# Performance work log

Hardware: AMD Instinct MI355X
Metric: run time of the kernel (lower is better)

The kernel has to match this reference:

```python
import jax, jax.numpy as jnp
import numpy as np

K = 1024
D = 256
BETA = 0.25


def setup_inputs() -> dict:
    key = jax.random.key(0)
    k1, k2 = jax.random.split(key)
    latents = jax.random.normal(k1, (32, D, 32, 32), dtype=jnp.float32)
    # nn.Embedding init: uniform(-1/K, 1/K)
    embedding = jax.random.uniform(k2, (K, D), dtype=jnp.float32,
                                   minval=-1.0 / K, maxval=1.0 / K)
    return {"latents": latents, "embedding": embedding}


def reference(latents, embedding):
    # latents: [B, D, H, W] -> [B, H, W, D]
    x = jnp.transpose(latents, (0, 2, 3, 1))
    input_shape = x.shape
    flat = x.reshape(-1, D)  # [N, D]

    # squared-L2 distances to codebook: [N, K]
    distances = (jnp.sum(flat ** 2, axis=1, keepdims=True)
                 + jnp.sum(embedding ** 2, axis=1)
                 - 2.0 * flat @ embedding.T)
    encoding_indices = jnp.argmin(distances, axis=1)  # [N]

    # one-hot encodings (returned output); quantize via direct gather
    encodings = jax.nn.one_hot(encoding_indices, K, dtype=latents.dtype)  # [N, K]
    quantized = embedding[encoding_indices].reshape(input_shape)  # [B, H, W, D]

    e_latent_loss = jnp.mean((jax.lax.stop_gradient(quantized) - x) ** 2)
    q_latent_loss = jnp.mean((quantized - jax.lax.stop_gradient(x)) ** 2)
    loss = q_latent_loss + BETA * e_latent_loss

    # straight-through estimator
    quantized_st = x + jax.lax.stop_gradient(quantized - x)

    avg_probs = jnp.mean(encodings, axis=0)  # [K]
    perplexity = jnp.exp(-jnp.sum(avg_probs * jnp.log(avg_probs + 1e-10)))

    return (loss,
            jnp.transpose(quantized_st, (0, 3, 1, 2)),  # [B, D, H, W]
            perplexity,
            encodings)
```

## Files before the change

kernel.cpp:

```cpp
#include <hip/hip_runtime.h>
#include <stdint.h>
#include <math.h>

typedef float  f32x4 __attribute__((ext_vector_type(4)));
typedef float  f32x2 __attribute__((ext_vector_type(2)));
typedef short  s16x8 __attribute__((ext_vector_type(8)));
typedef short  s16x4 __attribute__((ext_vector_type(4)));

#define KC   1024
#define DD   256
#define NR   32768

#define WS_HIST   0
#define WS_ACC    4096
#define WS_E2     8192
#define WS_IDX    12288
#define WS_PANEL  143360
#define WS_PART   671744

#define ENC_OFF   8388610ULL

#define A_OFF   0
#define B_OFF   32768
#define E2_OFF  49152
#define SMEM_SZ 51200

#define GLD16(gp, lp) __builtin_amdgcn_global_load_lds(                      \
    (const __attribute__((address_space(1))) uint32_t*)(gp),                 \
    (__attribute__((address_space(3))) uint32_t*)(lp), 16, 0, 0)

__device__ __forceinline__ short f2bf(float f) {
    uint32_t u = __builtin_bit_cast(uint32_t, f);
    uint32_t r = (u + 0x7FFFu + ((u >> 16) & 1u)) >> 16;
    return (short)r;
}

__global__ void k_prep(const float* __restrict__ emb, char* __restrict__ ws) {
    int tid = threadIdx.x;
    if (blockIdx.x == 0) {
        uint32_t* hist = (uint32_t*)(ws + WS_HIST);
        #pragma unroll
        for (int j = 0; j < 4; j++) hist[tid * 4 + j] = 0u;
        if (tid < 2) ((float*)(ws + WS_ACC))[tid] = 0.f;
    }
    int wid = tid >> 6, lane = tid & 63;
    int code = blockIdx.x * 4 + wid;
    const float* row = emb + (size_t)code * DD;
    f32x4 v = *(const f32x4*)(row + lane * 4);
    s16x4 b;
    b[0] = f2bf(v.x); b[1] = f2bf(v.y); b[2] = f2bf(v.z); b[3] = f2bf(v.w);
    *(s16x4*)((short*)(ws + WS_PANEL) + (size_t)code * DD + lane * 4) = b;
    float ss = v.x * v.x + v.y * v.y + v.z * v.z + v.w * v.w;
    #pragma unroll
    for (int off = 1; off < 64; off <<= 1) ss += __shfl_xor(ss, off);
    if (lane == 0) ((float*)(ws + WS_E2))[code] = ss;
}

__global__ __launch_bounds__(256, 2) void k_argmin(const float* __restrict__ latents,
                                                   char* __restrict__ ws) {
    const char*  panelb = (const char*)(ws + WS_PANEL);
    const float* e2g    = (const float*)(ws + WS_E2);
    float*       acc    = (float*)(ws + WS_ACC);

    __shared__ __align__(16) char smem[SMEM_SZ];

    int t     = threadIdx.x;
    int lane  = t & 63;
    int wid   = t >> 6;
    int g     = lane >> 4, r16 = lane & 15;
    int rowgrp = blockIdx.x >> 1;
    int chalf  = blockIdx.x & 1;
    int nbase  = rowgrp * 128;
    int b      = nbase >> 10;
    int hwbase = nbase & 1023;
    const char* pbase = panelb + (size_t)chalf * 262144;

    #pragma unroll
    for (int i = 0; i < 2; i++) {
        uint32_t off = i * 4096 + wid * 1024;
        uint32_t so  = off + lane * 16;
        uint32_t ssw = so ^ (((so >> 9) & 7u) << 4);
        GLD16(pbase + ssw, smem + B_OFF + off);
    }
    if (t < 128) {
        f32x4 ev = *(const f32x4*)(e2g + chalf * 512 + t * 4);
        *(f32x4*)(smem + E2_OFF + t * 16) = ev;
    }

    float xs = 0.f;
    s16x8 af[2][8];
    int rg = (t & 15) * 4;
    int dp = (t >> 4) * 2;
    int wb = 4 * ((t >> 4) & 3);

    #pragma unroll
    for (int h = 0; h < 2; h++) {
        const float* base = latents + (size_t)b * 262144 + hwbase + h * 64 + rg;
        #pragma unroll
        for (int i = 0; i < 8; i++) {
            int d = dp + i * 32;
            f32x4 v0 = *(const f32x4*)(base + (size_t)d * 1024);
            f32x4 v1 = *(const f32x4*)(base + (size_t)(d + 1) * 1024);
            xs += v0.x*v0.x + v0.y*v0.y + v0.z*v0.z + v0.w*v0.w;
            xs += v1.x*v1.x + v1.y*v1.y + v1.z*v1.z + v1.w*v1.w;
            int qb = d >> 3;
            #pragma unroll
            for (int q = 0; q < 4; q++) {
                int slot = rg + q;
                uint32_t pk = (uint32_t)(uint16_t)f2bf(v0[q])
                            | ((uint32_t)(uint16_t)f2bf(v1[q]) << 16);
                int quad = qb ^ (slot & 7);
                *(uint32_t*)(smem + A_OFF + slot * 512 + quad * 16 + wb) = pk;
            }
        }
        __syncthreads();
        if ((wid >> 1) == h) {
            int slotbase = (wid & 1) * 32;
            #pragma unroll
            for (int rt = 0; rt < 2; rt++) {
                #pragma unroll
                for (int kt = 0; kt < 8; kt++) {
                    int slot = slotbase + rt * 16 + r16;
                    int quad = (kt * 4 + g) ^ (slot & 7);
                    af[rt][kt] = *(const s16x8*)(smem + A_OFF + slot * 512 + quad * 16);
                }
            }
        }
        __syncthreads();
    }
    if (chalf == 0) {
        #pragma unroll
        for (int off = 1; off < 64; off <<= 1) xs += __shfl_xor(xs, off);
        if (lane == 0) atomicAdd(acc + 0, xs);
    }
    __syncthreads();

    float vmin[2][4];
    int   vidx[2][4];
    #pragma unroll
    for (int rt = 0; rt < 2; rt++)
        #pragma unroll
        for (int j = 0; j < 4; j++) { vmin[rt][j] = 3.4e38f; vidx[rt][j] = 0; }

    const float* E2l = (const float*)(smem + E2_OFF);
    int cur = 0;
    int codeglob = chalf * 512;
    for (int c = 0; c < 32; ++c) {
        if (c < 31) {
            size_t srcc = (size_t)(c + 1) * 8192;
            #pragma unroll
            for (int i = 0; i < 2; i++) {
                uint32_t off = i * 4096 + wid * 1024;
                uint32_t so  = off + lane * 16;
                uint32_t ssw = so ^ (((so >> 9) & 7u) << 4);
                GLD16(pbase + srcc + ssw, smem + B_OFF + (cur ^ 1) * 8192 + off);
            }
        }
        int cbase = c * 16;
        float e2c = E2l[cbase + r16];
        const char* Bc = smem + B_OFF + cur * 8192;
        s16x8 bf[8];
        #pragma unroll
        for (int kt = 0; kt < 8; kt++) {
            uint32_t byte = (uint32_t)(r16 * 512) + (((uint32_t)(kt * 64 + g * 16)) ^ (((uint32_t)(r16 & 7)) << 4));
            bf[kt] = *(const s16x8*)(Bc + byte);
        }
        #pragma unroll
        for (int rt = 0; rt < 2; rt++) {
            f32x4 a4 = {0.f, 0.f, 0.f, 0.f};
            #pragma unroll
            for (int kt = 0; kt < 8; kt++)
                a4 = __builtin_amdgcn_mfma_f32_16x16x32_bf16(af[rt][kt], bf[kt], a4, 0, 0, 0);
            #pragma unroll
            for (int j = 0; j < 4; j++) {
                float s = e2c - 2.f * a4[j];
                bool better = s < vmin[rt][j];
                vmin[rt][j] = better ? s : vmin[rt][j];
                vidx[rt][j] = better ? (codeglob + cbase + r16) : vidx[rt][j];
            }
        }
        __syncthreads();
        cur ^= 1;
    }

    uint2* part = (uint2*)(ws + WS_PART) + (size_t)chalf * NR;
    #pragma unroll
    for (int rt = 0; rt < 2; rt++) {
        #pragma unroll
        for (int j = 0; j < 4; j++) {
            float s = vmin[rt][j]; int ii = vidx[rt][j];
            #pragma unroll
            for (int off = 1; off < 16; off <<= 1) {
                float os = __shfl_xor(s, off);
                int   oi = __shfl_xor(ii, off);
                if (os < s || (os == s && oi < ii)) { s = os; ii = oi; }
            }
            if (r16 == 0) {
                int n = nbase + wid * 32 + rt * 16 + g * 4 + j;
                uint2 pv;
                pv.x = __builtin_bit_cast(uint32_t, s);
                pv.y = (uint32_t)ii;
                part[n] = pv;
            }
        }
    }
}

__global__ void k_comb(char* __restrict__ ws) {
    const uint2* part = (const uint2*)(ws + WS_PART);
    uint32_t* hist = (uint32_t*)(ws + WS_HIST);
    float*    acc  = (float*)(ws + WS_ACC);
    int*      idxo = (int*)(ws + WS_IDX);
    int n = blockIdx.x * 256 + threadIdx.x;
    uint2 p0 = part[n];
    uint2 p1 = part[NR + n];
    float s0 = __builtin_bit_cast(float, p0.x);
    float s1 = __builtin_bit_cast(float, p1.x);
    float s = (s1 < s0) ? s1 : s0;
    int  ii = (s1 < s0) ? (int)p1.y : (int)p0.y;
    idxo[n] = ii;
    atomicAdd(hist + ii, 1u);
    #pragma unroll
    for (int off = 1; off < 64; off <<= 1) s += __shfl_xor(s, off);
    if ((threadIdx.x & 63) == 0) atomicAdd(acc + 1, s);
}

__global__ void k_quant(const float* __restrict__ emb, const char* __restrict__ ws,
                        float* __restrict__ out) {
    const int* idx = (const int*)(ws + WS_IDX);
    int tid = threadIdx.x;
    int dg  = blockIdx.x & 63;
    int hwt = (blockIdx.x >> 6) & 3;
    int b   = blockIdx.x >> 8;
    int hw  = hwt * 256 + tid;
    int n   = b * 1024 + hw;
    int code = idx[n];
    f32x4 v = *(const f32x4*)(emb + (size_t)code * 256 + dg * 4);
    float* dst = out + 1 + (size_t)b * 262144 + (size_t)dg * 4096 + hw;
    dst[0] = v.x; dst[1024] = v.y; dst[2048] = v.z; dst[3072] = v.w;
}

__global__ void k_onehot(const char* __restrict__ ws, float* __restrict__ out) {
    const int* idx = (const int*)(ws + WS_IDX);
    __shared__ int lidx[8];
    int tid = threadIdx.x;
    int rbase = blockIdx.x * 8;
    if (tid < 8) lidx[tid] = idx[rbase + tid];
    __syncthreads();
    f32x2* enc = (f32x2*)(out + ENC_OFF);
    #pragma unroll
    for (int j = 0; j < 16; j++) {
        int linear = j * 256 + tid;
        int rl = linear >> 9, c2 = linear & 511;
        int id = lidx[rl];
        f32x2 v;
        v.x = (2 * c2     == id) ? 1.f : 0.f;
        v.y = (2 * c2 + 1 == id) ? 1.f : 0.f;
        enc[(size_t)(rbase + rl) * 512 + c2] = v;
    }
}

__global__ void k_final(const char* __restrict__ ws, float* __restrict__ out) {
    __shared__ float red[256];
    const uint32_t* hist = (const uint32_t*)(ws + WS_HIST);
    const float*    acc  = (const float*)(ws + WS_ACC);
    int tid = threadIdx.x;
    float part = 0.f;
    #pragma unroll
    for (int j = 0; j < 4; j++) {
        float p = (float)hist[tid * 4 + j] * (1.f / 32768.f);
        part += p * logf(p + 1e-10f);
    }
    red[tid] = part;
    __syncthreads();
    for (int s = 128; s > 0; s >>= 1) {
        if (tid < s) red[tid] += red[tid + s];
        __syncthreads();
    }
    if (tid == 0) {
        out[8388609] = expf(-red[0]);
        out[0] = 1.25f * (acc[0] + acc[1]) * (1.f / 8388608.f);
    }
}

extern "C" void kernel_launch(void* const* d_in, const int* in_sizes, int n_in,
                              void* d_out, int out_size, void* d_ws, size_t ws_size,
                              hipStream_t stream) {
    const float* latents = (const float*)d_in[0];
    const float* emb     = (const float*)d_in[1];
    float* out = (float*)d_out;
    char*  ws  = (char*)d_ws;

    hipLaunchKernelGGL(k_prep,   dim3(256),  dim3(256), 0, stream, emb, ws);
    hipLaunchKernelGGL(k_argmin, dim3(512),  dim3(256), 0, stream, latents, ws);
    hipLaunchKernelGGL(k_comb,   dim3(128),  dim3(256), 0, stream, ws);
    hipLaunchKernelGGL(k_quant,  dim3(8192), dim3(256), 0, stream, emb, ws, out);
    hipLaunchKernelGGL(k_onehot, dim3(4096), dim3(256), 0, stream, ws, out);
    hipLaunchKernelGGL(k_final,  dim3(1),    dim3(256), 0, stream, ws, out);
}
```

Before: 94.29 us.

## Deepen codebook panel staging to a four-buffer ring with manual vmcnt waits

Replaces the double-buffered codebook panel loop with a four-slot LDS ring that keeps three async global-to-LDS loads in flight. Each iteration uses explicit `s_waitcnt vmcnt` plus a single barrier, instead of a trailing `__syncthreads`. This is meant to hide global load latency behind the MFMA distance compute and cut barrier overhead. In exchange, LDS use grows by about 16KB, which may reduce occupancy. The first panel loads are also now issued only after the latent fragments are staged, rather than overlapping with them.

```diff
diff --git a/kernel.cpp b/kernel.cpp
--- a/kernel.cpp
+++ b/kernel.cpp
@@ -22,12 +22,16 @@
 
 #define A_OFF   0
 #define B_OFF   32768
-#define E2_OFF  49152
-#define SMEM_SZ 51200
+#define E2_OFF  65536
+#define SMEM_SZ 67584
 
 #define GLD16(gp, lp) __builtin_amdgcn_global_load_lds(                      \
     (const __attribute__((address_space(1))) uint32_t*)(gp),                 \
     (__attribute__((address_space(3))) uint32_t*)(lp), 16, 0, 0)
+
+#define WAITVM(N) asm volatile("s_waitcnt vmcnt(" #N ")" ::: "memory")
+#define PHASEBAR() do { __builtin_amdgcn_s_barrier();                        \
+                        __builtin_amdgcn_sched_barrier(0); } while (0)
 
 __device__ __forceinline__ short f2bf(float f) {
     uint32_t u = __builtin_bit_cast(uint32_t, f);
@@ -75,13 +79,6 @@
     int hwbase = nbase & 1023;
     const char* pbase = panelb + (size_t)chalf * 262144;
 
-    #pragma unroll
-    for (int i = 0; i < 2; i++) {
-        uint32_t off = i * 4096 + wid * 1024;
-        uint32_t so  = off + lane * 16;
-        uint32_t ssw = so ^ (((so >> 9) & 7u) << 4);
-        GLD16(pbase + ssw, smem + B_OFF + off);
-    }
     if (t < 128) {
         f32x4 ev = *(const f32x4*)(e2g + chalf * 512 + t * 4);
         *(f32x4*)(smem + E2_OFF + t * 16) = ev;
@@ -133,7 +130,6 @@
         for (int off = 1; off < 64; off <<= 1) xs += __shfl_xor(xs, off);
         if (lane == 0) atomicAdd(acc + 0, xs);
     }
-    __syncthreads();
 
     float vmin[2][4];
     int   vidx[2][4];
@@ -143,26 +139,28 @@
         for (int j = 0; j < 4; j++) { vmin[rt][j] = 3.4e38f; vidx[rt][j] = 0; }
 
     const float* E2l = (const float*)(smem + E2_OFF);
-    int cur = 0;
     int codeglob = chalf * 512;
-    for (int c = 0; c < 32; ++c) {
-        if (c < 31) {
-            size_t srcc = (size_t)(c + 1) * 8192;
-            #pragma unroll
-            for (int i = 0; i < 2; i++) {
-                uint32_t off = i * 4096 + wid * 1024;
-                uint32_t so  = off + lane * 16;
-                uint32_t ssw = so ^ (((so >> 9) & 7u) << 4);
-                GLD16(pbase + srcc + ssw, smem + B_OFF + (cur ^ 1) * 8192 + off);
-            }
-        }
+
+    auto stage = [&](int c) {
+        const char* srcc = pbase + (size_t)c * 8192;
+        char* dstb = smem + B_OFF + (size_t)(c & 3) * 8192;
+        #pragma unroll
+        for (int i = 0; i < 2; i++) {
+            uint32_t off = i * 4096 + wid * 1024;
+            uint32_t so  = off + lane * 16;
+            uint32_t ssw = so ^ (((so >> 9) & 7u) << 4);
+            GLD16(srcc + ssw, dstb + off);
+        }
+    };
+    auto compute = [&](int c) {
         int cbase = c * 16;
         float e2c = E2l[cbase + r16];
-        const char* Bc = smem + B_OFF + cur * 8192;
+        const char* Bc = smem + B_OFF + (size_t)(c & 3) * 8192;
         s16x8 bf[8];
         #pragma unroll
         for (int kt = 0; kt < 8; kt++) {
-            uint32_t byte = (uint32_t)(r16 * 512) + (((uint32_t)(kt * 64 + g * 16)) ^ (((uint32_t)(r16 & 7)) << 4));
+            uint32_t byte = (uint32_t)(r16 * 512)
+                          + (((uint32_t)(kt * 64 + g * 16)) ^ (((uint32_t)(r16 & 7)) << 4));
             bf[kt] = *(const s16x8*)(Bc + byte);
         }
         #pragma unroll
@@ -179,9 +177,19 @@
                 vidx[rt][j] = better ? (codeglob + cbase + r16) : vidx[rt][j];
             }
         }
-        __syncthreads();
-        cur ^= 1;
-    }
+    };
+
+    stage(0); stage(1); stage(2);
+    #pragma unroll 1
+    for (int c = 0; c < 29; ++c) {
+        WAITVM(4);
+        PHASEBAR();
+        compute(c);
+        stage(c + 3);
+    }
+    WAITVM(4); PHASEBAR(); compute(29);
+    WAITVM(2); PHASEBAR(); compute(30);
+    WAITVM(0); PHASEBAR(); compute(31);
 
     uint2* part = (uint2*)(ws + WS_PART) + (size_t)chalf * NR;
     #pragma unroll
```

After: 94.28 us. Within noise of the previous version (-0.0%).
